# Optimization experiments

Measured on AMD Instinct MI355X. Metric: run time of the kernel, lower is better.

Reference implementation:

```python
import jax, jax.numpy as jnp
import numpy as np

NUM_GROUPS = 32
EPS = 1e-6

def group_norm(x, gamma, beta):
    # x: (b, c, h, w)
    b, c, h, w = x.shape
    xg = x.reshape(b, NUM_GROUPS, c // NUM_GROUPS, h, w)
    mean = xg.mean(axis=(2, 3, 4), keepdims=True)
    var = xg.var(axis=(2, 3, 4), keepdims=True)
    xn = ((xg - mean) * jax.lax.rsqrt(var + EPS)).reshape(b, c, h, w)
    return xn * gamma[None, :, None, None] + beta[None, :, None, None]

def conv1x1(x, W, bias):
    # W: (out_c, in_c); 1x1 conv == channel matmul
    return jnp.einsum('oc,bchw->bohw', W, x) + bias[None, :, None, None]

def setup_inputs() -> dict:
    key = jax.random.key(0)
    ks = jax.random.split(key, 11)
    C = 512
    x = jax.random.normal(ks[0], (4, C, 64, 64), dtype=jnp.float32)
    s = 1.0 / np.sqrt(C)
    d = {
        'x': x,
        'gamma': jnp.ones((C,), jnp.float32),
        'beta': jnp.zeros((C,), jnp.float32),
        'Wq': jax.random.normal(ks[1], (C, C), jnp.float32) * s,
        'bq': jax.random.normal(ks[2], (C,), jnp.float32) * 0.01,
        'Wk': jax.random.normal(ks[3], (C, C), jnp.float32) * s,
        'bk': jax.random.normal(ks[4], (C,), jnp.float32) * 0.01,
        'Wv': jax.random.normal(ks[5], (C, C), jnp.float32) * s,
        'bv': jax.random.normal(ks[6], (C,), jnp.float32) * 0.01,
        'Wp': jax.random.normal(ks[7], (C, C), jnp.float32) * s,
        'bp': jax.random.normal(ks[8], (C,), jnp.float32) * 0.01,
    }
    return d

def reference(x, gamma, beta, Wq, bq, Wk, bk, Wv, bv, Wp, bp):
    b, c, h, w = x.shape
    hn = group_norm(x, gamma, beta)
    q = conv1x1(hn, Wq, bq).reshape(b, c, h * w)  # (b,c,n)
    k = conv1x1(hn, Wk, bk).reshape(b, c, h * w)
    v = conv1x1(hn, Wv, bv).reshape(b, c, h * w)
    scale = jnp.asarray(c, x.dtype) ** -0.5
    # scores[b,m,n] = sum_c q[b,c,m] * k[b,c,n]
    scores = jnp.einsum('bcm,bcn->bmn', q, k) * scale
    attn = jax.nn.softmax(scores, axis=2)  # softmax over key positions n
    # h_[b,c,m] = sum_n v[b,c,n] * attn[b,m,n]
    out = jnp.einsum('bcn,bmn->bcm', v, attn).reshape(b, c, h, w)
    return x + conv1x1(out, Wp, bp)
```

## Files before the change

kernel.cpp:

```cpp
#include <hip/hip_runtime.h>
#include <math.h>


#define BATCH 4
#define CH    512
#define NPOS  4096
#define NGRP  32
#define GSIZE (16 * NPOS)
#define WSZ   262144
#define KVB   64
#define NT    64

typedef __attribute__((ext_vector_type(8))) short bf16x8;
typedef __attribute__((ext_vector_type(4))) float f32x4;

__device__ __forceinline__ ushort f2b(float x) {
    uint u = __float_as_uint(x);
    u += 0x7fff + ((u >> 16) & 1);
    return (ushort)(u >> 16);
}

__device__ __forceinline__ void gld16(void* lds, const void* g) {
    __builtin_amdgcn_global_load_lds(
        (const __attribute__((address_space(1))) void*)g,
        (__attribute__((address_space(3))) void*)lds, 16, 0, 0);
}

__global__ __launch_bounds__(256) void prep_k(
    const float* __restrict__ x, float* __restrict__ stats,
    const float* __restrict__ Wq, const float* __restrict__ Wk,
    const float* __restrict__ Wv, const float* __restrict__ Wp,
    ushort* __restrict__ W4) {
    if (blockIdx.x >= 128) {
        int id = blockIdx.x - 128;
        int sel = id >> 7, blk = id & 127;
        const float* src = sel == 0 ? Wq : (sel == 1 ? Wk : (sel == 2 ? Wv : Wp));
        const float4* s4 = (const float4*)(src + (size_t)blk * 2048);
        ushort4* d4 = (ushort4*)(W4 + (size_t)sel * WSZ + (size_t)blk * 2048);
        for (int i = threadIdx.x; i < 512; i += 256) {
            float4 v = s4[i];
            d4[i] = make_ushort4(f2b(v.x), f2b(v.y), f2b(v.z), f2b(v.w));
        }
        return;
    }
    int bg = blockIdx.x;
    const float4* xp = reinterpret_cast<const float4*>(x + (size_t)bg * GSIZE);
    float s1 = 0.f, s2 = 0.f;
    for (int i = threadIdx.x; i < GSIZE / 4; i += 256) {
        float4 v = xp[i];
        s1 += v.x + v.y + v.z + v.w;
        s2 += v.x * v.x + v.y * v.y + v.z * v.z + v.w * v.w;
    }
    for (int off = 32; off > 0; off >>= 1) {
        s1 += __shfl_down(s1, off);
        s2 += __shfl_down(s2, off);
    }
    __shared__ float r1[4], r2[4];
    int wid = threadIdx.x >> 6;
    if ((threadIdx.x & 63) == 0) { r1[wid] = s1; r2[wid] = s2; }
    __syncthreads();
    if (threadIdx.x == 0) {
        float t1 = r1[0] + r1[1] + r1[2] + r1[3];
        float t2 = r2[0] + r2[1] + r2[2] + r2[3];
        float mean = t1 / (float)GSIZE;
        float var  = t2 / (float)GSIZE - mean * mean;
        stats[bg]       = mean;
        stats[128 + bg] = rsqrtf(var + 1e-6f);
    }
}

__global__ __launch_bounds__(256) void hnT_k(
    const float* __restrict__ x, const float* __restrict__ gamma,
    const float* __restrict__ beta, const float* __restrict__ stats,
    ushort* __restrict__ hnT) {
    int bm = blockIdx.x * 64, c0 = blockIdx.y * 64, b = blockIdx.z;
    __shared__ ushort Ls[64][65];
    int t = threadIdx.x, tx = t & 15, ty = t >> 4;
    const float* xb = x + ((size_t)b * CH + c0) * NPOS + bm;
#pragma unroll
    for (int it = 0; it < 4; ++it) {
        int cc = ty + it * 16;
        int ch = c0 + cc;
        int bg = b * NGRP + (ch >> 4);
        float ga = stats[128 + bg] * gamma[ch];
        float be = beta[ch] - stats[bg] * ga;
        float4 v = *(const float4*)(xb + (size_t)cc * NPOS + tx * 4);
        Ls[cc][tx * 4 + 0] = f2b(v.x * ga + be);
        Ls[cc][tx * 4 + 1] = f2b(v.y * ga + be);
        Ls[cc][tx * 4 + 2] = f2b(v.z * ga + be);
        Ls[cc][tx * 4 + 3] = f2b(v.w * ga + be);
    }
    __syncthreads();
#pragma unroll
    for (int it = 0; it < 4; ++it) {
        int mm = ty + it * 16;
        ushort4 o;
        o.x = Ls[tx * 4 + 0][mm];
        o.y = Ls[tx * 4 + 1][mm];
        o.z = Ls[tx * 4 + 2][mm];
        o.w = Ls[tx * 4 + 3][mm];
        *(ushort4*)(hnT + ((size_t)(b * NPOS) + bm + mm) * CH + c0 + tx * 4) = o;
    }
}

__global__ __launch_bounds__(256) void qkv3_k(
    const ushort* __restrict__ hnT, const ushort* __restrict__ W4,
    const float* __restrict__ bq, const float* __restrict__ bk,
    const float* __restrict__ bv,
    ushort* __restrict__ qT, ushort* __restrict__ kT, ushort* __restrict__ vB) {
    int bm = blockIdx.x * 64, bo = blockIdx.y * 64, b = blockIdx.z;
    int t = threadIdx.x, l = t & 63, w = t >> 6;
    int wr = w & 1, wc = w >> 1;
    int lr = l & 15, lg = l >> 4;

    const ushort* ha  = hnT + ((size_t)(b * NPOS) + bm + wr * 32 + lr) * CH + lg * 8;
    const ushort* wqp = W4 + (size_t)(bo + wc * 32 + lr) * CH + lg * 8;
    const ushort* wkp = wqp + WSZ;
    const ushort* wvp = wkp + WSZ;

    f32x4 aq[2][2], ak[2][2], av[2][2];
#pragma unroll
    for (int i = 0; i < 2; ++i)
#pragma unroll
        for (int j = 0; j < 2; ++j) {
            aq[i][j] = (f32x4){0.f, 0.f, 0.f, 0.f};
            ak[i][j] = (f32x4){0.f, 0.f, 0.f, 0.f};
            av[i][j] = (f32x4){0.f, 0.f, 0.f, 0.f};
        }
    bf16x8 a0 = *(const bf16x8*)(ha);
    bf16x8 a1 = *(const bf16x8*)(ha + 16 * CH);
    bf16x8 q0 = *(const bf16x8*)(wqp);
    bf16x8 q1 = *(const bf16x8*)(wqp + 16 * CH);
    bf16x8 k0 = *(const bf16x8*)(wkp);
    bf16x8 k1 = *(const bf16x8*)(wkp + 16 * CH);
    bf16x8 v0 = *(const bf16x8*)(wvp);
    bf16x8 v1 = *(const bf16x8*)(wvp + 16 * CH);
#pragma unroll
    for (int s = 0; s < 16; ++s) {
        bf16x8 na0, na1, nq0, nq1, nk0, nk1, nv0, nv1;
        if (s < 15) {
            int c1 = (s + 1) * 32;
            na0 = *(const bf16x8*)(ha + c1);
            na1 = *(const bf16x8*)(ha + 16 * CH + c1);
            nq0 = *(const bf16x8*)(wqp + c1);
            nq1 = *(const bf16x8*)(wqp + 16 * CH + c1);
            nk0 = *(const bf16x8*)(wkp + c1);
            nk1 = *(const bf16x8*)(wkp + 16 * CH + c1);
            nv0 = *(const bf16x8*)(wvp + c1);
            nv1 = *(const bf16x8*)(wvp + 16 * CH + c1);
        }
        aq[0][0] = __builtin_amdgcn_mfma_f32_16x16x32_bf16(a0, q0, aq[0][0], 0, 0, 0);
        aq[0][1] = __builtin_amdgcn_mfma_f32_16x16x32_bf16(a0, q1, aq[0][1], 0, 0, 0);
        aq[1][0] = __builtin_amdgcn_mfma_f32_16x16x32_bf16(a1, q0, aq[1][0], 0, 0, 0);
        aq[1][1] = __builtin_amdgcn_mfma_f32_16x16x32_bf16(a1, q1, aq[1][1], 0, 0, 0);
        ak[0][0] = __builtin_amdgcn_mfma_f32_16x16x32_bf16(a0, k0, ak[0][0], 0, 0, 0);
        ak[0][1] = __builtin_amdgcn_mfma_f32_16x16x32_bf16(a0, k1, ak[0][1], 0, 0, 0);
        ak[1][0] = __builtin_amdgcn_mfma_f32_16x16x32_bf16(a1, k0, ak[1][0], 0, 0, 0);
        ak[1][1] = __builtin_amdgcn_mfma_f32_16x16x32_bf16(a1, k1, ak[1][1], 0, 0, 0);
        av[0][0] = __builtin_amdgcn_mfma_f32_16x16x32_bf16(v0, a0, av[0][0], 0, 0, 0);
        av[0][1] = __builtin_amdgcn_mfma_f32_16x16x32_bf16(v0, a1, av[0][1], 0, 0, 0);
        av[1][0] = __builtin_amdgcn_mfma_f32_16x16x32_bf16(v1, a0, av[1][0], 0, 0, 0);
        av[1][1] = __builtin_amdgcn_mfma_f32_16x16x32_bf16(v1, a1, av[1][1], 0, 0, 0);
        if (s < 15) {
            a0 = na0; a1 = na1; q0 = nq0; q1 = nq1;
            k0 = nk0; k1 = nk1; v0 = nv0; v1 = nv1;
        }
    }
    const float sc = 0.044194173824159216f;
#pragma unroll
    for (int j = 0; j < 2; ++j) {
        int o = bo + wc * 32 + j * 16 + lr;
        float bqv = bq[o], bkv = bk[o];
#pragma unroll
        for (int i = 0; i < 2; ++i)
#pragma unroll
            for (int r = 0; r < 4; ++r) {
                int m = bm + wr * 32 + i * 16 + 4 * lg + r;
                size_t base = ((size_t)(b * NPOS) + m) * CH + o;
                qT[base] = f2b((aq[i][j][r] + bqv) * sc);
                kT[base] = f2b(ak[i][j][r] + bkv);
            }
    }
#pragma unroll
    for (int i = 0; i < 2; ++i)
#pragma unroll
        for (int r = 0; r < 4; ++r) {
            int o = bo + wc * 32 + i * 16 + 4 * lg + r;
            float bvv = bv[o];
#pragma unroll
            for (int j = 0; j < 2; ++j) {
                int m = bm + wr * 32 + j * 16 + lr;
                vB[((size_t)(b * CH) + o) * NPOS + m] = f2b(av[i][j][r] + bvv);
            }
        }
}

__global__ __launch_bounds__(512) __attribute__((amdgpu_waves_per_eu(2, 2)))
void attn_k(
    const ushort* __restrict__ qT, const ushort* __restrict__ kT,
    const ushort* __restrict__ vB, ushort* __restrict__ aoT) {
    __shared__ ushort Ks[KVB * 512];
    __shared__ ushort Vs[512 * KVB];
    __shared__ ushort P_lds[64 * 72];
    __shared__ float mpart[2][4][16];

    int id = blockIdx.x;
    int b  = (id & 7) >> 1;
    int mt = ((id >> 3) << 1) | (id & 1);
    int m0 = mt * 64;

    int t = threadIdx.x, l = t & 63, w = t >> 6;
    int mi = w & 3, ci = w >> 2;
    int lr = l & 15, lg = l >> 4;

    const ushort* kTb = kT + (size_t)b * NPOS * CH;
    const ushort* vBb = vB + (size_t)b * CH * NPOS;

    auto stageK = [&](int n0) {
#pragma unroll
        for (int i = 0; i < 8; ++i) {
            int n = w * 8 + i;
            const ushort* g = kTb + (size_t)(n0 + n) * CH + (l ^ (n & 7)) * 8;
            gld16(&Ks[n * 512], g);
        }
    };
    auto stageV = [&](int n0) {
#pragma unroll
        for (int i = 0; i < 8; ++i) {
            int cb = w * 64 + i * 8;
            int c  = cb + (l >> 3);
            int sc = (l & 7) ^ (c & 7);
            const ushort* g = vBb + (size_t)c * NPOS + n0 + sc * 8;
            gld16(&Vs[cb * KVB], g);
        }
    };

    stageK(0);

    const ushort* qrow = qT + ((size_t)(b * NPOS + m0 + mi * 16 + lr)) * CH + lg * 8;
    bf16x8 qf[16];
#pragma unroll
    for (int ks = 0; ks < 16; ++ks) qf[ks] = *(const bf16x8*)(qrow + ks * 32);

    f32x4 acc[16];
#pragma unroll
    for (int i = 0; i < 16; ++i) acc[i] = (f32x4){0.f, 0.f, 0.f, 0.f};
    float m_run[4], lsum[4];
#pragma unroll
    for (int r = 0; r < 4; ++r) { m_run[r] = -1e30f; lsum[r] = 0.f; }

    int zk = lr & 7;
    for (int nt = 0; nt < NT; ++nt) {
        int n0 = nt * KVB;
        asm volatile("s_waitcnt vmcnt(0)" ::: "memory");
        __builtin_amdgcn_s_barrier();
        __builtin_amdgcn_sched_barrier(0);
        stageV(n0);
        f32x4 s0a = {0.f, 0.f, 0.f, 0.f}, s0b = s0a, s1a = s0a, s1b = s0a;
        const ushort* krow0 = &Ks[(ci * 32 + lr) * 512];
        const ushort* krow1 = &Ks[(ci * 32 + 16 + lr) * 512];
#pragma unroll
        for (int ks = 0; ks < 16; ks += 2) {
            bf16x8 k0a = *(const bf16x8*)(krow0 + (((ks + 0) * 4 + lg) ^ zk) * 8);
            bf16x8 k0b = *(const bf16x8*)(krow0 + (((ks + 1) * 4 + lg) ^ zk) * 8);
            bf16x8 k1a = *(const bf16x8*)(krow1 + (((ks + 0) * 4 + lg) ^ zk) * 8);
            bf16x8 k1b = *(const bf16x8*)(krow1 + (((ks + 1) * 4 + lg) ^ zk) * 8);
            s0a = __builtin_amdgcn_mfma_f32_16x16x32_bf16(qf[ks + 0], k0a, s0a, 0, 0, 0);
            s0b = __builtin_amdgcn_mfma_f32_16x16x32_bf16(qf[ks + 1], k0b, s0b, 0, 0, 0);
            s1a = __builtin_amdgcn_mfma_f32_16x16x32_bf16(qf[ks + 0], k1a, s1a, 0, 0, 0);
            s1b = __builtin_amdgcn_mfma_f32_16x16x32_bf16(qf[ks + 1], k1b, s1b, 0, 0, 0);
        }
        f32x4 s0 = s0a + s0b;
        f32x4 s1 = s1a + s1b;
        float pm[4];
#pragma unroll
        for (int r = 0; r < 4; ++r) pm[r] = fmaxf(s0[r], s1[r]);
#pragma unroll
        for (int off = 1; off < 16; off <<= 1)
#pragma unroll
            for (int r = 0; r < 4; ++r) pm[r] = fmaxf(pm[r], __shfl_xor(pm[r], off));
        if (lr == 0) {
#pragma unroll
            for (int r = 0; r < 4; ++r) mpart[ci][mi][4 * lg + r] = pm[r];
        }
        asm volatile("s_waitcnt lgkmcnt(0)" ::: "memory");
        __builtin_amdgcn_s_barrier();
        __builtin_amdgcn_sched_barrier(0);
        if (nt + 1 < NT) stageK((nt + 1) * KVB);
        float mt2[4];
        float growth = -1e30f;
#pragma unroll
        for (int r = 0; r < 4; ++r) {
            int row = 4 * lg + r;
            mt2[r] = fmaxf(mpart[0][mi][row], mpart[1][mi][row]);
            growth = fmaxf(growth, mt2[r] - m_run[r]);
        }
        bool resc = !__all(growth <= 8.0f);
        if (resc) {
            float alpha[4];
#pragma unroll
            for (int r = 0; r < 4; ++r) {
                float mnew = fmaxf(m_run[r], mt2[r]);
                alpha[r] = __expf(m_run[r] - mnew);
                m_run[r] = mnew;
                lsum[r] *= alpha[r];
            }
#pragma unroll
            for (int cs = 0; cs < 16; ++cs) {
                acc[cs][0] *= alpha[0]; acc[cs][1] *= alpha[1];
                acc[cs][2] *= alpha[2]; acc[cs][3] *= alpha[3];
            }
        }
        float p0[4], p1[4];
#pragma unroll
        for (int r = 0; r < 4; ++r) {
            p0[r] = __expf(s0[r] - m_run[r]);
            p1[r] = __expf(s1[r] - m_run[r]);
            lsum[r] += p0[r] + p1[r];
        }
#pragma unroll
        for (int r = 0; r < 4; ++r) {
            int row = mi * 16 + 4 * lg + r;
            P_lds[row * 72 + ci * 32 + lr]      = f2b(p0[r]);
            P_lds[row * 72 + ci * 32 + 16 + lr] = f2b(p1[r]);
        }
        if (nt + 1 < NT) {
            asm volatile("s_waitcnt vmcnt(8)" ::: "memory");
        } else {
            asm volatile("s_waitcnt vmcnt(0)" ::: "memory");
        }
        asm volatile("s_waitcnt lgkmcnt(0)" ::: "memory");
        __builtin_amdgcn_s_barrier();
        __builtin_amdgcn_sched_barrier(0);
        bf16x8 pa0 = *(const bf16x8*)&P_lds[(mi * 16 + lr) * 72 + lg * 8];
        bf16x8 pa1 = *(const bf16x8*)&P_lds[(mi * 16 + lr) * 72 + 32 + lg * 8];
#pragma unroll
        for (int cs = 0; cs < 16; ++cs) {
            int c = ci * 256 + cs * 16 + lr;
            bf16x8 vf0 = *(const bf16x8*)&Vs[c * KVB + (((0 * 4 + lg) ^ (c & 7)) * 8)];
            bf16x8 vf1 = *(const bf16x8*)&Vs[c * KVB + (((1 * 4 + lg) ^ (c & 7)) * 8)];
            acc[cs] = __builtin_amdgcn_mfma_f32_16x16x32_bf16(pa0, vf0, acc[cs], 0, 0, 0);
            acc[cs] = __builtin_amdgcn_mfma_f32_16x16x32_bf16(pa1, vf1, acc[cs], 0, 0, 0);
        }
    }
    float ls[4];
#pragma unroll
    for (int r = 0; r < 4; ++r) ls[r] = lsum[r];
#pragma unroll
    for (int off = 1; off < 16; off <<= 1)
#pragma unroll
        for (int r = 0; r < 4; ++r) ls[r] += __shfl_xor(ls[r], off);
    if (lr == 0) {
#pragma unroll
        for (int r = 0; r < 4; ++r) mpart[ci][mi][4 * lg + r] = ls[r];
    }
    asm volatile("s_waitcnt lgkmcnt(0)" ::: "memory");
    __builtin_amdgcn_s_barrier();
    __builtin_amdgcn_sched_barrier(0);
    float inv[4];
#pragma unroll
    for (int r = 0; r < 4; ++r) {
        int row = 4 * lg + r;
        inv[r] = 1.0f / (mpart[0][mi][row] + mpart[1][mi][row]);
    }
#pragma unroll
    for (int cs = 0; cs < 16; ++cs)
#pragma unroll
        for (int r = 0; r < 4; ++r)
            aoT[((size_t)(b * NPOS + m0 + mi * 16 + 4 * lg + r)) * CH
                + ci * 256 + cs * 16 + lr] = f2b(acc[cs][r] * inv[r]);
}

__global__ __launch_bounds__(256) void proj_k(
    const ushort* __restrict__ aoT, const ushort* __restrict__ W4,
    const float* __restrict__ bp, const float* __restrict__ x,
    float* __restrict__ out) {
    int bm = blockIdx.x * 64, bo = blockIdx.y * 64, b = blockIdx.z;
    int t = threadIdx.x, l = t & 63, w = t >> 6;
    int orh = w & 1, mc = w >> 1;
    int lr = l & 15, lg = l >> 4;

    const ushort* wp = W4 + 3 * (size_t)WSZ + (size_t)(bo + orh * 32 + lr) * CH + lg * 8;
    const ushort* ab = aoT + ((size_t)(b * NPOS) + bm + mc * 32 + lr) * CH + lg * 8;

    f32x4 ac[2][2];
#pragma unroll
    for (int i = 0; i < 2; ++i)
#pragma unroll
        for (int j = 0; j < 2; ++j) ac[i][j] = (f32x4){0.f, 0.f, 0.f, 0.f};
    bf16x8 w0 = *(const bf16x8*)(wp);
    bf16x8 w1 = *(const bf16x8*)(wp + 16 * CH);
    bf16x8 b0 = *(const bf16x8*)(ab);
    bf16x8 b1 = *(const bf16x8*)(ab + 16 * CH);
#pragma unroll
    for (int s = 0; s < 16; ++s) {
        bf16x8 nw0, nw1, nb0, nb1;
        if (s < 15) {
            int c1 = (s + 1) * 32;
            nw0 = *(const bf16x8*)(wp + c1);
            nw1 = *(const bf16x8*)(wp + 16 * CH + c1);
            nb0 = *(const bf16x8*)(ab + c1);
            nb1 = *(const bf16x8*)(ab + 16 * CH + c1);
        }
        ac[0][0] = __builtin_amdgcn_mfma_f32_16x16x32_bf16(w0, b0, ac[0][0], 0, 0, 0);
        ac[0][1] = __builtin_amdgcn_mfma_f32_16x16x32_bf16(w0, b1, ac[0][1], 0, 0, 0);
        ac[1][0] = __builtin_amdgcn_mfma_f32_16x16x32_bf16(w1, b0, ac[1][0], 0, 0, 0);
        ac[1][1] = __builtin_amdgcn_mfma_f32_16x16x32_bf16(w1, b1, ac[1][1], 0, 0, 0);
        if (s < 15) { w0 = nw0; w1 = nw1; b0 = nb0; b1 = nb1; }
    }
#pragma unroll
    for (int i = 0; i < 2; ++i)
#pragma unroll
        for (int r = 0; r < 4; ++r) {
            int o = bo + orh * 32 + i * 16 + 4 * lg + r;
            float bpv = bp[o];
#pragma unroll
            for (int j = 0; j < 2; ++j) {
                int m = bm + mc * 32 + j * 16 + lr;
                size_t base = ((size_t)(b * CH) + o) * NPOS + m;
                out[base] = ac[i][j][r] + bpv + x[base];
            }
        }
}

extern "C" void kernel_launch(void* const* d_in, const int* in_sizes, int n_in,
                              void* d_out, int out_size, void* d_ws, size_t ws_size,
                              hipStream_t stream) {
    const float* x     = (const float*)d_in[0];
    const float* gamma = (const float*)d_in[1];
    const float* beta  = (const float*)d_in[2];
    const float* Wq    = (const float*)d_in[3];
    const float* bq    = (const float*)d_in[4];
    const float* Wk    = (const float*)d_in[5];
    const float* bk    = (const float*)d_in[6];
    const float* Wv    = (const float*)d_in[7];
    const float* bv    = (const float*)d_in[8];
    const float* Wp    = (const float*)d_in[9];
    const float* bp    = (const float*)d_in[10];
    float* out = (float*)d_out;

    const size_t SZ = (size_t)BATCH * CH * NPOS;
    const size_t need = (5 * SZ + 4 * WSZ) * 2 + 1024;
    if (ws_size < need) return;

    ushort* qT  = (ushort*)d_ws;
    ushort* kT  = qT + SZ;
    ushort* vb  = kT + SZ;
    ushort* hnT = vb + SZ;
    ushort* aoT = hnT + SZ;
    ushort* W4  = aoT + SZ;
    float*  stats = (float*)(W4 + 4 * (size_t)WSZ);

    prep_k<<<640, 256, 0, stream>>>(x, stats, Wq, Wk, Wv, Wp, W4);
    hnT_k<<<dim3(64, 8, 4), 256, 0, stream>>>(x, gamma, beta, stats, hnT);
    qkv3_k<<<dim3(64, 8, 4), 256, 0, stream>>>(hnT, W4, bq, bk, bv, qT, kT, vb);
    attn_k<<<dim3(256), 512, 0, stream>>>(qT, kT, vb, aoT);
    proj_k<<<dim3(64, 8, 4), 256, 0, stream>>>(aoT, W4, bp, x, out);
}
```

Baseline: 424.5 us.

## Retile PV stage so each wave reuses V fragments across two row tiles

In the attention kernel, each wave now computes a 32-row by 128-channel slice of the PV product instead of 16 rows by 256 channels. Each V fragment read from LDS feeds two MFMAs, which halves V shared-memory traffic per MFMA. Because a wave's output rows no longer match the rows it computed scores for, it keeps a separate running max for its PV rows, derived from the shared partial maxima. The lazy rescale with a threshold is replaced by an unconditional rescale every tile. That adds exponentials and 64 accumulator multiplies per wave per tile.

```diff
diff --git a/kernel.cpp b/kernel.cpp
--- a/kernel.cpp
+++ b/kernel.cpp
@@ -211,6 +211,7 @@
 
     int t = threadIdx.x, l = t & 63, w = t >> 6;
     int mi = w & 3, ci = w >> 2;
+    int pm = w & 1, pc = w >> 1;
     int lr = l & 15, lg = l >> 4;
 
     const ushort* kTb = kT + (size_t)b * NPOS * CH;
@@ -242,12 +243,18 @@
 #pragma unroll
     for (int ks = 0; ks < 16; ++ks) qf[ks] = *(const bf16x8*)(qrow + ks * 32);
 
-    f32x4 acc[16];
-#pragma unroll
-    for (int i = 0; i < 16; ++i) acc[i] = (f32x4){0.f, 0.f, 0.f, 0.f};
-    float m_run[4], lsum[4];
-#pragma unroll
-    for (int r = 0; r < 4; ++r) { m_run[r] = -1e30f; lsum[r] = 0.f; }
+    f32x4 acc0[8], acc1[8];
+#pragma unroll
+    for (int i = 0; i < 8; ++i) {
+        acc0[i] = (f32x4){0.f, 0.f, 0.f, 0.f};
+        acc1[i] = (f32x4){0.f, 0.f, 0.f, 0.f};
+    }
+    float m_run[4], lsum[4], m_pv0[4], m_pv1[4];
+#pragma unroll
+    for (int r = 0; r < 4; ++r) {
+        m_run[r] = -1e30f; lsum[r] = 0.f;
+        m_pv0[r] = -1e30f; m_pv1[r] = -1e30f;
+    }
 
     int zk = lr & 7;
     for (int nt = 0; nt < NT; ++nt) {
@@ -272,57 +279,61 @@
         }
         f32x4 s0 = s0a + s0b;
         f32x4 s1 = s1a + s1b;
-        float pm[4];
-#pragma unroll
-        for (int r = 0; r < 4; ++r) pm[r] = fmaxf(s0[r], s1[r]);
+        float pm_[4];
+#pragma unroll
+        for (int r = 0; r < 4; ++r) pm_[r] = fmaxf(s0[r], s1[r]);
 #pragma unroll
         for (int off = 1; off < 16; off <<= 1)
 #pragma unroll
-            for (int r = 0; r < 4; ++r) pm[r] = fmaxf(pm[r], __shfl_xor(pm[r], off));
+            for (int r = 0; r < 4; ++r) pm_[r] = fmaxf(pm_[r], __shfl_xor(pm_[r], off));
         if (lr == 0) {
 #pragma unroll
-            for (int r = 0; r < 4; ++r) mpart[ci][mi][4 * lg + r] = pm[r];
+            for (int r = 0; r < 4; ++r) mpart[ci][mi][4 * lg + r] = pm_[r];
         }
         asm volatile("s_waitcnt lgkmcnt(0)" ::: "memory");
         __builtin_amdgcn_s_barrier();
         __builtin_amdgcn_sched_barrier(0);
         if (nt + 1 < NT) stageK((nt + 1) * KVB);
-        float mt2[4];
-        float growth = -1e30f;
+        float aqk[4], p0[4], p1[4];
 #pragma unroll
         for (int r = 0; r < 4; ++r) {
             int row = 4 * lg + r;
-            mt2[r] = fmaxf(mpart[0][mi][row], mpart[1][mi][row]);
-            growth = fmaxf(growth, mt2[r] - m_run[r]);
-        }
-        bool resc = !__all(growth <= 8.0f);
-        if (resc) {
-            float alpha[4];
-#pragma unroll
-            for (int r = 0; r < 4; ++r) {
-                float mnew = fmaxf(m_run[r], mt2[r]);
-                alpha[r] = __expf(m_run[r] - mnew);
-                m_run[r] = mnew;
-                lsum[r] *= alpha[r];
-            }
-#pragma unroll
-            for (int cs = 0; cs < 16; ++cs) {
-                acc[cs][0] *= alpha[0]; acc[cs][1] *= alpha[1];
-                acc[cs][2] *= alpha[2]; acc[cs][3] *= alpha[3];
-            }
-        }
-        float p0[4], p1[4];
+            float mt2 = fmaxf(mpart[0][mi][row], mpart[1][mi][row]);
+            float mnew = fmaxf(m_run[r], mt2);
+            aqk[r] = __expf(m_run[r] - mnew);
+            m_run[r] = mnew;
+        }
 #pragma unroll
         for (int r = 0; r < 4; ++r) {
             p0[r] = __expf(s0[r] - m_run[r]);
             p1[r] = __expf(s1[r] - m_run[r]);
-            lsum[r] += p0[r] + p1[r];
+            lsum[r] = lsum[r] * aqk[r] + p0[r] + p1[r];
         }
 #pragma unroll
         for (int r = 0; r < 4; ++r) {
             int row = mi * 16 + 4 * lg + r;
             P_lds[row * 72 + ci * 32 + lr]      = f2b(p0[r]);
             P_lds[row * 72 + ci * 32 + 16 + lr] = f2b(p1[r]);
+        }
+        float apv0[4], apv1[4];
+#pragma unroll
+        for (int r = 0; r < 4; ++r) {
+            int row = 4 * lg + r;
+            float ma = fmaxf(mpart[0][pm * 2][row], mpart[1][pm * 2][row]);
+            float na = fmaxf(m_pv0[r], ma);
+            apv0[r] = __expf(m_pv0[r] - na);
+            m_pv0[r] = na;
+            float mb = fmaxf(mpart[0][pm * 2 + 1][row], mpart[1][pm * 2 + 1][row]);
+            float nb = fmaxf(m_pv1[r], mb);
+            apv1[r] = __expf(m_pv1[r] - nb);
+            m_pv1[r] = nb;
+        }
+#pragma unroll
+        for (int cs = 0; cs < 8; ++cs) {
+            acc0[cs][0] *= apv0[0]; acc0[cs][1] *= apv0[1];
+            acc0[cs][2] *= apv0[2]; acc0[cs][3] *= apv0[3];
+            acc1[cs][0] *= apv1[0]; acc1[cs][1] *= apv1[1];
+            acc1[cs][2] *= apv1[2]; acc1[cs][3] *= apv1[3];
         }
         if (nt + 1 < NT) {
             asm volatile("s_waitcnt vmcnt(8)" ::: "memory");
@@ -332,15 +343,21 @@
         asm volatile("s_waitcnt lgkmcnt(0)" ::: "memory");
         __builtin_amdgcn_s_barrier();
         __builtin_amdgcn_sched_barrier(0);
-        bf16x8 pa0 = *(const bf16x8*)&P_lds[(mi * 16 + lr) * 72 + lg * 8];
-        bf16x8 pa1 = *(const bf16x8*)&P_lds[(mi * 16 + lr) * 72 + 32 + lg * 8];
-#pragma unroll
-        for (int cs = 0; cs < 16; ++cs) {
-            int c = ci * 256 + cs * 16 + lr;
+        int prow0 = (pm * 32 + lr) * 72;
+        int prow1 = (pm * 32 + 16 + lr) * 72;
+        bf16x8 pa00 = *(const bf16x8*)&P_lds[prow0 + lg * 8];
+        bf16x8 pa01 = *(const bf16x8*)&P_lds[prow0 + 32 + lg * 8];
+        bf16x8 pa10 = *(const bf16x8*)&P_lds[prow1 + lg * 8];
+        bf16x8 pa11 = *(const bf16x8*)&P_lds[prow1 + 32 + lg * 8];
+#pragma unroll
+        for (int cs = 0; cs < 8; ++cs) {
+            int c = pc * 128 + cs * 16 + lr;
             bf16x8 vf0 = *(const bf16x8*)&Vs[c * KVB + (((0 * 4 + lg) ^ (c & 7)) * 8)];
             bf16x8 vf1 = *(const bf16x8*)&Vs[c * KVB + (((1 * 4 + lg) ^ (c & 7)) * 8)];
-            acc[cs] = __builtin_amdgcn_mfma_f32_16x16x32_bf16(pa0, vf0, acc[cs], 0, 0, 0);
-            acc[cs] = __builtin_amdgcn_mfma_f32_16x16x32_bf16(pa1, vf1, acc[cs], 0, 0, 0);
+            acc0[cs] = __builtin_amdgcn_mfma_f32_16x16x32_bf16(pa00, vf0, acc0[cs], 0, 0, 0);
+            acc0[cs] = __builtin_amdgcn_mfma_f32_16x16x32_bf16(pa01, vf1, acc0[cs], 0, 0, 0);
+            acc1[cs] = __builtin_amdgcn_mfma_f32_16x16x32_bf16(pa10, vf0, acc1[cs], 0, 0, 0);
+            acc1[cs] = __builtin_amdgcn_mfma_f32_16x16x32_bf16(pa11, vf1, acc1[cs], 0, 0, 0);
         }
     }
     float ls[4];
@@ -357,18 +374,22 @@
     asm volatile("s_waitcnt lgkmcnt(0)" ::: "memory");
     __builtin_amdgcn_s_barrier();
     __builtin_amdgcn_sched_barrier(0);
-    float inv[4];
+    float inv0[4], inv1[4];
 #pragma unroll
     for (int r = 0; r < 4; ++r) {
         int row = 4 * lg + r;
-        inv[r] = 1.0f / (mpart[0][mi][row] + mpart[1][mi][row]);
-    }
-#pragma unroll
-    for (int cs = 0; cs < 16; ++cs)
-#pragma unroll
-        for (int r = 0; r < 4; ++r)
-            aoT[((size_t)(b * NPOS + m0 + mi * 16 + 4 * lg + r)) * CH
-                + ci * 256 + cs * 16 + lr] = f2b(acc[cs][r] * inv[r]);
+        inv0[r] = 1.0f / (mpart[0][pm * 2][row] + mpart[1][pm * 2][row]);
+        inv1[r] = 1.0f / (mpart[0][pm * 2 + 1][row] + mpart[1][pm * 2 + 1][row]);
+    }
+#pragma unroll
+    for (int cs = 0; cs < 8; ++cs)
+#pragma unroll
+        for (int r = 0; r < 4; ++r) {
+            size_t ro = (size_t)(b * NPOS + m0 + pm * 32 + 4 * lg + r);
+            int col = pc * 128 + cs * 16 + lr;
+            aoT[ro * CH + col]        = f2b(acc0[cs][r] * inv0[r]);
+            aoT[(ro + 16) * CH + col] = f2b(acc1[cs][r] * inv1[r]);
+        }
 }
 
 __global__ __launch_bounds__(256) void proj_k(
```

Result: slower. 489.0 us (+15.2%).
